# Kernel tuning notes

Measured on AMD Instinct MI355X. Metric: run time of the kernel, lower is better.

Reference implementation:

```python
import jax, jax.numpy as jnp
import numpy as np

N_NODES = 50000
N_EDGES = 800000
NUM_GRAPHS = 128
KS = 5           # kernel_size per pseudo dim
K = KS * KS      # 25 spline weight matrices per layer


def spline_coeff(pseudo):
    """Open linear (degree-1) B-spline basis for 2-D pseudo coords in [0,1].
    Returns dense per-edge coefficients over the K=25 kernel slots: [E, K]."""
    pos = pseudo * (KS - 1)                      # [E,2]
    lo = jnp.clip(jnp.floor(pos).astype(jnp.int32), 0, KS - 2)
    frac = pos - lo.astype(pseudo.dtype)         # [E,2]
    i0, i1 = lo, lo + 1
    w0, w1 = 1.0 - frac, frac
    # 2^dim = 4 corner combinations, flat index = d0 + KS*d1
    idx = jnp.stack([i0[:, 0] + KS * i0[:, 1],
                     i0[:, 0] + KS * i1[:, 1],
                     i1[:, 0] + KS * i0[:, 1],
                     i1[:, 0] + KS * i1[:, 1]], axis=1)            # [E,4]
    w = jnp.stack([w0[:, 0] * w0[:, 1], w0[:, 0] * w1[:, 1],
                   w1[:, 0] * w0[:, 1], w1[:, 0] * w1[:, 1]], axis=1)  # [E,4]
    E = pseudo.shape[0]
    coeff = jnp.zeros((E, K), pseudo.dtype).at[jnp.arange(E)[:, None], idx].add(w)
    return coeff


def spline_conv(x, coeff, src, dst, W, root, bias):
    """SplineConv: gather src feats, spline-weighted transform, scatter-mean to dst,
    plus root weight and bias. x:[N,in], coeff:[E,K], W:[K,in,out]."""
    n = x.shape[0]
    x_src = x[src]                                # [E,in] gather
    m = coeff[:, 0:1] * (x_src @ W[0])            # [E,out]
    for k in range(1, K):                         # fixed small loop over K kernels
        m = m + coeff[:, k:k + 1] * (x_src @ W[k])
    agg = jax.ops.segment_sum(m, dst, num_segments=n)
    cnt = jax.ops.segment_sum(jnp.ones((src.shape[0],), x.dtype), dst, num_segments=n)
    agg = agg / jnp.maximum(cnt, 1.0)[:, None]    # mean aggregation (PyG default)
    return agg + x @ root + bias


def setup_inputs() -> dict:
    key = jax.random.key(0)
    ks = jax.random.split(key, 16)
    s = 0.1  # small init scale for numerical stability
    return {
        "x": jax.random.normal(ks[0], (N_NODES, 1), jnp.float32),
        "position": jax.random.uniform(ks[1], (N_NODES, 2), jnp.float32),
        "pseudo": jax.random.uniform(ks[2], (N_EDGES, 2), jnp.float32),
        "edge_index": jax.random.randint(ks[3], (2, N_EDGES), 0, N_NODES, jnp.int32),
        "batch": jnp.sort(jax.random.randint(ks[4], (N_NODES,), 0, NUM_GRAPHS, jnp.int32)),
        "W1": s * jax.random.normal(ks[5], (K, 1, 32), jnp.float32),
        "root1": s * jax.random.normal(ks[6], (1, 32), jnp.float32),
        "b1": jnp.zeros((32,), jnp.float32),
        "W2": s * jax.random.normal(ks[7], (K, 32, 64), jnp.float32),
        "root2": s * jax.random.normal(ks[8], (32, 64), jnp.float32),
        "b2": jnp.zeros((64,), jnp.float32),
        "W3": s * jax.random.normal(ks[9], (K, 64, 64), jnp.float32),
        "root3": s * jax.random.normal(ks[10], (64, 64), jnp.float32),
        "b3": jnp.zeros((64,), jnp.float32),
        "fc_w": s * jax.random.normal(ks[11], (64, 10), jnp.float32),
        "fc_b": jnp.zeros((10,), jnp.float32),
    }


def reference(x, position, pseudo, edge_index, batch,
              W1, root1, b1, W2, root2, b2, W3, root3, b3, fc_w, fc_b):
    # `position` is accepted but unused, matching the original forward.
    src, dst = edge_index[0], edge_index[1]
    coeff = spline_coeff(pseudo)
    h = jax.nn.elu(spline_conv(x, coeff, src, dst, W1, root1, b1))
    h = jax.nn.elu(spline_conv(h, coeff, src, dst, W2, root2, b2))
    h = jax.nn.elu(spline_conv(h, coeff, src, dst, W3, root3, b3))
    # scatter_mean pooling over batch indices -> [NUM_GRAPHS, 64]
    pooled = jax.ops.segment_sum(h, batch, num_segments=NUM_GRAPHS)
    gcnt = jax.ops.segment_sum(jnp.ones((h.shape[0],), h.dtype), batch,
                               num_segments=NUM_GRAPHS)
    pooled = pooled / jnp.maximum(gcnt, 1.0)[:, None]
    # dropout is identity in eval mode
    logits = pooled @ fc_w + fc_b
    return jax.nn.log_softmax(logits, axis=1)
```

## Files before the change

### kernel.cpp

```cpp
#include <hip/hip_runtime.h>

#define NN 50000
#define NE 800000
#define NG 128
#define NB_SCAN 196
#define PADW 0xC1000000u

typedef unsigned int uint;
typedef unsigned short ushort;
typedef __attribute__((ext_vector_type(8))) short short8;
typedef __attribute__((ext_vector_type(4))) float f32x4;
typedef __attribute__((ext_vector_type(16))) float f32x16;

__device__ __forceinline__ float bf2f(ushort u){ union{uint i; float f;} v; v.i=(uint)u<<16; return v.f; }
__device__ __forceinline__ ushort f2bf(float f){ union{float f; uint i;} v; v.f=f; return (ushort)((v.i + 0x7FFFu + ((v.i>>16)&1u))>>16); }
__device__ __forceinline__ int iswz(int i){ return i ^ ((i>>4)&3); }

__global__ void zero_k(int* hist, float* pooled, int* gcnt){
    int i = blockIdx.x*blockDim.x + threadIdx.x;
    if (i < NN) hist[i] = 0;
    if (i < NG*64) pooled[i] = 0.f;
    if (i < NG) gcnt[i] = 0;
}

__global__ void hist_k(const int* __restrict__ ei, int* __restrict__ hist){
    int e = blockIdx.x*blockDim.x + threadIdx.x;
    if (e < NE) atomicAdd(&hist[ei[NE + e]], 1);
}

__global__ __launch_bounds__(256) void scan1(const int* __restrict__ hist, int* __restrict__ bsum){
    __shared__ int sm[256];
    int t = threadIdx.x, i = blockIdx.x*256 + t;
    sm[t] = (i < NN) ? hist[i] : 0;
    __syncthreads();
    for (int o = 128; o > 0; o >>= 1){ if (t < o) sm[t] += sm[t+o]; __syncthreads(); }
    if (t == 0) bsum[blockIdx.x] = sm[0];
}
__global__ __launch_bounds__(256) void scan2(const int* __restrict__ bsum, int* __restrict__ bpre){
    __shared__ int sm[256];
    int t = threadIdx.x;
    int v = (t < NB_SCAN) ? bsum[t] : 0;
    sm[t] = v; __syncthreads();
    int acc = v;
    for (int o = 1; o < 256; o <<= 1){
        int u = (t >= o) ? sm[t-o] : 0; __syncthreads();
        acc += u; sm[t] = acc; __syncthreads();
    }
    if (t < NB_SCAN) bpre[t] = acc - v;
}
__global__ __launch_bounds__(256) void scan3(const int* __restrict__ hist, const int* __restrict__ bpre,
                                             int* __restrict__ offs, int* __restrict__ cursor,
                                             float* __restrict__ invc){
    __shared__ int sm[256];
    int t = threadIdx.x, b = blockIdx.x, i = b*256 + t;
    int v = (i < NN) ? hist[i] : 0;
    sm[t] = v; __syncthreads();
    int acc = v;
    for (int o = 1; o < 256; o <<= 1){
        int u = (t >= o) ? sm[t-o] : 0; __syncthreads();
        acc += u; sm[t] = acc; __syncthreads();
    }
    int excl = acc - v + bpre[b];
    if (i < NN){ offs[i] = excl; cursor[i] = excl; invc[i] = 1.0f/(float)max(v,1); }
    if (i == NN-1) offs[NN] = NE;
}

__global__ void scatter_k(const int* __restrict__ ei, const float* __restrict__ pseudo,
                          int* __restrict__ cursor, uint4* __restrict__ payA){
    int e = blockIdx.x*blockDim.x + threadIdx.x;
    if (e >= NE) return;
    float2 ps = *(const float2*)(pseudo + 2*(size_t)e);
    float px = ps.x * 4.0f, py = ps.y * 4.0f;
    int lx = min(max((int)floorf(px), 0), 3);
    int ly = min(max((int)floorf(py), 0), 3);
    uint meta = (uint)ei[e] | ((uint)lx<<16) | ((uint)ly<<18);
    int pos = atomicAdd(&cursor[ei[NE + e]], 1);
    payA[pos] = make_uint4(meta, __float_as_uint(px), __float_as_uint(py), 0u);
}

template<int IN>
__global__ void wprep_k(const float* __restrict__ W, const float* __restrict__ root, ushort* __restrict__ Bp){
    const int total = 26*IN*64;
    int tid = blockIdx.x*blockDim.x + threadIdx.x;
    if (tid >= total) return;
    int j    = tid & 7;
    int lane = (tid >> 3) & 63;
    int ctkt = tid >> 9;
    int ct   = ctkt & 3;
    int kt   = ctkt >> 2;
    int kk   = kt*32 + (lane>>4)*8 + j;
    int col  = ct*16 + (lane & 15);
    float v;
    if (kk < 25*IN){ int k = kk / IN; int i = kk % IN; v = W[((size_t)k*IN + i)*64 + col]; }
    else           { v = root[(size_t)(kk - 25*IN)*64 + col]; }
    Bp[tid] = f2bf(v);
}

__global__ __launch_bounds__(256) void reduce1_k(const float* __restrict__ x, const uint4* __restrict__ payA,
                                                 const int* __restrict__ offs, const float* __restrict__ invc,
                                                 const float* __restrict__ W1, const float* __restrict__ root1,
                                                 const float* __restrict__ b1, ushort* __restrict__ h1bf){
    __shared__ float w1s[25*32];
    for (int i = threadIdx.x; i < 25*32; i += 256) w1s[i] = W1[i];
    __syncthreads();
    int wid  = threadIdx.x >> 6;
    int lane = threadIdx.x & 63;
    int o    = lane & 31;
    int half = lane >> 5;
    int d    = blockIdx.x*4 + wid;
    int s = offs[d], e = offs[d+1];
    float acc = 0.f;
#define E1(QA, XS) { uint meta = (QA).x; \
    int lx = (meta>>16)&3, ly = (meta>>18)&3; \
    float px = __uint_as_float((QA).y), py = __uint_as_float((QA).z); \
    float fx = px - (float)lx, fy = py - (float)ly; \
    float gx = 1.f - fx, gy = 1.f - fy; \
    float wa = half ? fx*gy : gx*gy; \
    float wb = half ? fx*fy : gx*fy; \
    int ka = ly*5 + lx + half; \
    acc += (wa*w1s[ka*32 + o] + wb*w1s[(ka+5)*32 + o]) * (XS); }
    int p = s;
    for (; p + 4 <= e; p += 4){
        uint4 a0 = payA[p], a1 = payA[p+1], a2 = payA[p+2], a3 = payA[p+3];
        float x0 = x[a0.x & 0xFFFF], x1 = x[a1.x & 0xFFFF];
        float x2 = x[a2.x & 0xFFFF], x3 = x[a3.x & 0xFFFF];
        E1(a0, x0) E1(a1, x1) E1(a2, x2) E1(a3, x3)
    }
    for (; p < e; ++p){
        uint4 a0 = payA[p];
        float x0 = x[a0.x & 0xFFFF];
        E1(a0, x0)
    }
#undef E1
    acc += __shfl_xor(acc, 32);
    if (half == 0){
        float val = acc*invc[d] + x[d]*root1[o] + b1[o];
        val = val > 0.f ? val : expm1f(val);
        h1bf[(size_t)d*32 + o] = f2bf(val);
    }
}

#define WCALC(Q0, AH, AL) { \
    float px_ = __uint_as_float((Q0).y), py_ = __uint_as_float((Q0).z); \
    float wx_ = fmaxf(1.f - fabsf(px_ - fi0), 0.f); \
    float wy_ = fmaxf(1.f - fabsf(py_ - fj0), 0.f); \
    float wv_ = wx_ * wy_; \
    uint wb_ = __float_as_uint(wv_); \
    (AH) = (short)(ushort)(wb_ >> 16); \
    float hif_ = __uint_as_float(wb_ & 0xFFFF0000u); \
    (AL) = (short)(ushort)(__float_as_uint(wv_ - hif_) >> 16); }

template<int MODE>
__global__ __launch_bounds__(512) void fused32(
        const ushort* __restrict__ hin, const uint4* __restrict__ payA,
        const int* __restrict__ offs, const float* __restrict__ invc,
        const ushort* __restrict__ Bp, const float* __restrict__ bias,
        const int* __restrict__ batch, ushort* __restrict__ hout,
        float* __restrict__ pooled, int* __restrict__ gcnt)
{
    constexpr int KT = 26, KH = 13;
    __shared__ __align__(16) ushort Sb[KT*512];
    __shared__ __align__(16) uint4 eA[8][16];
    __shared__ float red[1024];
    __shared__ float outS[1024];

    const int tid = threadIdx.x, lane = tid & 63, w = tid >> 6;
    const int ln31 = lane & 31, kg2 = lane >> 5;
    const int d0 = blockIdx.x * 16;
    const float fi0 = (float)(ln31 % 5), fj0 = (float)(ln31 / 5);
    const uint4 PAD4 = make_uint4(0u, PADW, PADW, 0u);

    for (int nn = 0; nn < 2; ++nn){
        const int node = w*2 + nn;
        const int d = d0 + node;
        int s = offs[d];
        int h = offs[d+1] - s;
        int steps = (h + 15) >> 4;

        f32x16 accH;
        #pragma unroll
        for (int q = 0; q < 16; ++q) accH[q] = 0.f;

        uint4 vA = PAD4;
        {
            int rem = (h < 16) ? h : 16;
            if (lane < rem) vA = payA[(size_t)s + lane];
        }
        for (int ks = 0; ks < steps; ++ks){
            if (lane < 16) eA[w][lane] = vA;
            if (ks+1 < steps){
                int rem = h - (ks+1)*16; if (rem > 16) rem = 16;
                uint4 nA = PAD4;
                if (lane < rem) nA = payA[(size_t)(s + (ks+1)*16) + lane];
                vA = nA;
            }
            short8 ah, al;
            uint srcs[8];
            #pragma unroll
            for (int j = 0; j < 8; ++j){
                uint4 q0 = eA[w][kg2*8 + j];
                WCALC(q0, ah[j], al[j])
                srcs[j] = q0.x & 0xFFFFu;
            }
            short8 bfv;
            #pragma unroll
            for (int j = 0; j < 8; ++j)
                bfv[j] = (short)hin[(size_t)srcs[j]*32 + ln31];
            accH = __builtin_amdgcn_mfma_f32_32x32x16_bf16(ah, bfv, accH, 0, 0, 0);
            accH = __builtin_amdgcn_mfma_f32_32x32x16_bf16(al, bfv, accH, 0, 0, 0);
        }

        {
            float ic = invc[d];
            int jd  = ln31 & 7;
            int l3  = ln31 >> 3;
            #pragma unroll
            for (int reg = 0; reg < 16; ++reg){
                int r = (reg & 3) + 8*(reg >> 2) + 4*kg2;
                if (r < 25)
                    Sb[r*512 + iswz(l3*16 + node)*8 + jd] = f2bf(accH[reg]*ic);
            }
            if (lane < 32)
                Sb[25*512 + iswz(((lane>>3)&3)*16 + node)*8 + (lane&7)] = hin[(size_t)d*32 + lane];
        }
    }
    __syncthreads();

    {
        int ct = w & 3, kh = w >> 2;
        int c15 = lane & 15, kg = lane >> 4;
        int ig = iswz(lane);
        f32x4 a4 = {0.f,0.f,0.f,0.f};
        const ushort* bb = Bp + ct*512 + (size_t)lane*8;
        #pragma unroll
        for (int k = 0; k < KH; ++k){
            int kt = kh*KH + k;
            short8 a = *(const short8*)(Sb + kt*512 + ig*8);
            short8 b = *(const short8*)(bb + (size_t)kt*2048);
            a4 = __builtin_amdgcn_mfma_f32_16x16x32_bf16(a, b, a4, 0, 0, 0);
        }
        if (kh == 1){
            float* rr = red + (ct*64 + lane)*4;
            rr[0]=a4[0]; rr[1]=a4[1]; rr[2]=a4[2]; rr[3]=a4[3];
        }
        __syncthreads();
        if (kh == 0){
            const float* rr = red + (ct*64 + lane)*4;
            int col = ct*16 + c15;
            float bs = bias[col];
            #pragma unroll
            for (int jq = 0; jq < 4; ++jq){
                int r16 = kg*4 + jq;
                float v = a4[jq] + rr[jq] + bs;
                v = v > 0.f ? v : expm1f(v);
                if (MODE == 0) ((ushort*)outS)[r16*64 + col] = f2bf(v);
                else           outS[r16*64 + col] = v;
            }
        }
    }
    __syncthreads();

    if (MODE == 0){
        uint* dst = (uint*)(hout + (size_t)d0*64);
        dst[tid] = ((const uint*)outS)[tid];
    } else {
        if (w == 0){
            int c = lane;
            float run = 0.f; int gprev = batch[d0];
            for (int r = 0; r < 16; ++r){
                int g = batch[d0 + r];
                if (g != gprev){ atomicAdd(&pooled[gprev*64 + c], run); run = 0.f; gprev = g; }
                run += outS[r*64 + c];
            }
            atomicAdd(&pooled[gprev*64 + c], run);
        } else if (w == 1 && lane == 0){
            int cnt = 0; int gprev = batch[d0];
            for (int r = 0; r < 16; ++r){
                int g = batch[d0 + r];
                if (g != gprev){ atomicAdd(&gcnt[gprev], cnt); cnt = 0; gprev = g; }
                cnt++;
            }
            atomicAdd(&gcnt[gprev], cnt);
        }
    }
}

template<int MODE>
__global__ __launch_bounds__(512) void fused64(
        const ushort* __restrict__ hin, const uint4* __restrict__ payA,
        const int* __restrict__ offs, const float* __restrict__ invc,
        const ushort* __restrict__ Bp, const float* __restrict__ bias,
        const int* __restrict__ batch, ushort* __restrict__ hout,
        float* __restrict__ pooled, int* __restrict__ gcnt)
{
    constexpr int KT = 52, KH = 26;
    __shared__ __align__(16) ushort Sb[KT*512];
    __shared__ __align__(16) uint4 eA[8][16];
    __shared__ float red[1024];
    __shared__ float outS[1024];

    const int tid = threadIdx.x, lane = tid & 63, w = tid >> 6;
    const int ln31 = lane & 31, kg2 = lane >> 5;
    const int d0 = blockIdx.x * 16;
    const float fi0 = (float)(ln31 % 5), fj0 = (float)(ln31 / 5);
    const uint4 PAD4 = make_uint4(0u, PADW, PADW, 0u);

    for (int nn = 0; nn < 2; ++nn){
        const int node = w*2 + nn;
        const int d = d0 + node;
        int s = offs[d];
        int h = offs[d+1] - s;
        int steps = (h + 15) >> 4;

        f32x16 acc0, acc1;
        #pragma unroll
        for (int q = 0; q < 16; ++q){ acc0[q] = 0.f; acc1[q] = 0.f; }

        uint4 vA = PAD4;
        {
            int rem = (h < 16) ? h : 16;
            if (lane < rem) vA = payA[(size_t)s + lane];
        }
        for (int ks = 0; ks < steps; ++ks){
            if (lane < 16) eA[w][lane] = vA;
            if (ks+1 < steps){
                int rem = h - (ks+1)*16; if (rem > 16) rem = 16;
                uint4 nA = PAD4;
                if (lane < rem) nA = payA[(size_t)(s + (ks+1)*16) + lane];
                vA = nA;
            }
            short8 ah, al;
            uint hx[8];
            #pragma unroll
            for (int j = 0; j < 8; ++j){
                uint4 q0 = eA[w][kg2*8 + j];
                WCALC(q0, ah[j], al[j])
                hx[j] = *(const uint*)(hin + (size_t)(q0.x & 0xFFFFu)*64 + 2*ln31);
            }
            short8 b0, b1;
            #pragma unroll
            for (int j = 0; j < 8; ++j){
                b0[j] = (short)(ushort)hx[j];
                b1[j] = (short)(ushort)(hx[j] >> 16);
            }
            acc0 = __builtin_amdgcn_mfma_f32_32x32x16_bf16(ah, b0, acc0, 0, 0, 0);
            acc0 = __builtin_amdgcn_mfma_f32_32x32x16_bf16(al, b0, acc0, 0, 0, 0);
            acc1 = __builtin_amdgcn_mfma_f32_32x32x16_bf16(ah, b1, acc1, 0, 0, 0);
            acc1 = __builtin_amdgcn_mfma_f32_32x32x16_bf16(al, b1, acc1, 0, 0, 0);
        }

        {
            float ic = invc[d];
            int off0 = 2*ln31;
            int fhi  = ln31 >> 4;
            int kgp  = (off0 >> 3) & 3;
            int jd0  = off0 & 7;
            int gsl  = iswz(kgp*16 + node)*8;
            #pragma unroll
            for (int reg = 0; reg < 16; ++reg){
                int r = (reg & 3) + 8*(reg >> 2) + 4*kg2;
                if (r < 25){
                    int kt = r*2 + fhi;
                    uint pk = (uint)f2bf(acc0[reg]*ic) | ((uint)f2bf(acc1[reg]*ic) << 16);
                    *(uint*)(Sb + kt*512 + gsl + jd0) = pk;
                }
            }
            int f = lane;
            Sb[(50 + (f>>5))*512 + iswz(((f>>3)&3)*16 + node)*8 + (f&7)] = hin[(size_t)d*64 + f];
        }
    }
    __syncthreads();

    {
        int ct = w & 3, kh = w >> 2;
        int c15 = lane & 15, kg = lane >> 4;
        int ig = iswz(lane);
        f32x4 a4 = {0.f,0.f,0.f,0.f};
        const ushort* bb = Bp + ct*512 + (size_t)lane*8;
        #pragma unroll
        for (int k = 0; k < KH; ++k){
            int kt = kh*KH + k;
            short8 a = *(const short8*)(Sb + kt*512 + ig*8);
            short8 b = *(const short8*)(bb + (size_t)kt*2048);
            a4 = __builtin_amdgcn_mfma_f32_16x16x32_bf16(a, b, a4, 0, 0, 0);
        }
        if (kh == 1){
            float* rr = red + (ct*64 + lane)*4;
            rr[0]=a4[0]; rr[1]=a4[1]; rr[2]=a4[2]; rr[3]=a4[3];
        }
        __syncthreads();
        if (kh == 0){
            const float* rr = red + (ct*64 + lane)*4;
            int col = ct*16 + c15;
            float bs = bias[col];
            #pragma unroll
            for (int jq = 0; jq < 4; ++jq){
                int r16 = kg*4 + jq;
                float v = a4[jq] + rr[jq] + bs;
                v = v > 0.f ? v : expm1f(v);
                if (MODE == 0) ((ushort*)outS)[r16*64 + col] = f2bf(v);
                else           outS[r16*64 + col] = v;
            }
        }
    }
    __syncthreads();

    if (MODE == 0){
        uint* dst = (uint*)(hout + (size_t)d0*64);
        dst[tid] = ((const uint*)outS)[tid];
    } else {
        if (w == 0){
            int c = lane;
            float run = 0.f; int gprev = batch[d0];
            for (int r = 0; r < 16; ++r){
                int g = batch[d0 + r];
                if (g != gprev){ atomicAdd(&pooled[gprev*64 + c], run); run = 0.f; gprev = g; }
                run += outS[r*64 + c];
            }
            atomicAdd(&pooled[gprev*64 + c], run);
        } else if (w == 1 && lane == 0){
            int cnt = 0; int gprev = batch[d0];
            for (int r = 0; r < 16; ++r){
                int g = batch[d0 + r];
                if (g != gprev){ atomicAdd(&gcnt[gprev], cnt); cnt = 0; gprev = g; }
                cnt++;
            }
            atomicAdd(&gcnt[gprev], cnt);
        }
    }
}

__global__ __launch_bounds__(128) void head_k(const float* __restrict__ pooled, const int* __restrict__ gcnt,
                                              const float* __restrict__ fcw, const float* __restrict__ fcb,
                                              float* __restrict__ out){
    int g = threadIdx.x;
    if (g >= NG) return;
    float inv = 1.0f / fmaxf((float)gcnt[g], 1.0f);
    float logits[10];
    #pragma unroll
    for (int c = 0; c < 10; ++c) logits[c] = fcb[c];
    for (int o = 0; o < 64; ++o){
        float m = pooled[g*64 + o] * inv;
        #pragma unroll
        for (int c = 0; c < 10; ++c) logits[c] += m * fcw[o*10 + c];
    }
    float mx = logits[0];
    #pragma unroll
    for (int c = 1; c < 10; ++c) mx = fmaxf(mx, logits[c]);
    float ssum = 0.f;
    #pragma unroll
    for (int c = 0; c < 10; ++c) ssum += expf(logits[c] - mx);
    float lse = logf(ssum) + mx;
    #pragma unroll
    for (int c = 0; c < 10; ++c) out[g*10 + c] = logits[c] - lse;
}

extern "C" void kernel_launch(void* const* d_in, const int* in_sizes, int n_in,
                              void* d_out, int out_size, void* d_ws, size_t ws_size,
                              hipStream_t stream) {
    const float* x      = (const float*)d_in[0];
    const float* pseudo = (const float*)d_in[2];
    const int*   ei     = (const int*)  d_in[3];
    const int*   batch  = (const int*)  d_in[4];
    const float* W1     = (const float*)d_in[5];
    const float* root1  = (const float*)d_in[6];
    const float* b1     = (const float*)d_in[7];
    const float* W2     = (const float*)d_in[8];
    const float* root2  = (const float*)d_in[9];
    const float* b2     = (const float*)d_in[10];
    const float* W3     = (const float*)d_in[11];
    const float* root3  = (const float*)d_in[12];
    const float* b3     = (const float*)d_in[13];
    const float* fcw    = (const float*)d_in[14];
    const float* fcb    = (const float*)d_in[15];
    float* out = (float*)d_out;

    char* ws = (char*)d_ws;
    size_t off = 0;
    auto alloc = [&](size_t bytes)->char*{ char* p = ws + off; off += (bytes + 255) / 256 * 256; return p; };
    uint4*  payA   = (uint4*) alloc((size_t)NE*16);
    ushort* h1bf   = (ushort*)alloc((size_t)NN*32*2);
    ushort* h2bf   = (ushort*)alloc((size_t)NN*64*2);
    int*    hist   = (int*)   alloc((size_t)NN*4);
    int*    offs   = (int*)   alloc((size_t)(NN+1)*4);
    int*    cursor = (int*)   alloc((size_t)NN*4);
    float*  invc   = (float*) alloc((size_t)NN*4);
    int*    bsum   = (int*)   alloc((size_t)NB_SCAN*4);
    int*    bpre   = (int*)   alloc((size_t)NB_SCAN*4);
    ushort* Bp2    = (ushort*)alloc((size_t)26*2048*2);
    ushort* Bp3    = (ushort*)alloc((size_t)52*2048*2);
    float*  pooled = (float*) alloc((size_t)NG*64*4);
    int*    gcnt   = (int*)   alloc((size_t)NG*4);
    (void)ws_size; (void)in_sizes; (void)n_in; (void)out_size;

    zero_k   <<<NB_SCAN, 256, 0, stream>>>(hist, pooled, gcnt);
    hist_k   <<<(NE+255)/256, 256, 0, stream>>>(ei, hist);
    scan1    <<<NB_SCAN, 256, 0, stream>>>(hist, bsum);
    scan2    <<<1, 256, 0, stream>>>(bsum, bpre);
    scan3    <<<NB_SCAN, 256, 0, stream>>>(hist, bpre, offs, cursor, invc);
    scatter_k<<<(NE+255)/256, 256, 0, stream>>>(ei, pseudo, cursor, payA);
    wprep_k<32><<<(26*32*64 + 255)/256, 256, 0, stream>>>(W2, root2, Bp2);
    wprep_k<64><<<(26*64*64 + 255)/256, 256, 0, stream>>>(W3, root3, Bp3);
    reduce1_k<<<NN/4, 256, 0, stream>>>(x, payA, offs, invc, W1, root1, b1, h1bf);
    fused32<0><<<NN/16, 512, 0, stream>>>(h1bf, payA, offs, invc, Bp2, b2, batch, h2bf, pooled, gcnt);
    fused64<1><<<NN/16, 512, 0, stream>>>(h2bf, payA, offs, invc, Bp3, b3, batch, h2bf, pooled, gcnt);
    head_k   <<<1, 128, 0, stream>>>(pooled, gcnt, fcw, fcb, out);
}
```

Before: 280.3 us.

## Double-buffer edge payload via direct global-to-LDS async loads

Replaces the register-staged edge payload prefetch with global_load_lds DMA into a double-buffered LDS array per wave. The next 16-edge chunk is issued before processing the current one, with explicit vmcnt waits and a scheduling barrier. The goal is to drop the register round-trip and the LDS store, and to overlap payload fetch with the gather and MFMA work. The manual waitcnt and the lack of explicit LDS visibility sync add correctness risk, and the sched_barrier may limit compiler interleaving of the gather loads.

```diff
diff --git a/kernel.cpp b/kernel.cpp
--- a/kernel.cpp
+++ b/kernel.cpp
@@ -150,6 +150,15 @@
     float hif_ = __uint_as_float(wb_ & 0xFFFF0000u); \
     (AL) = (short)(ushort)(__float_as_uint(wv_ - hif_) >> 16); }
 
+#define STAGE(BUF, STEP) { \
+    int rem_ = h - (STEP)*16; if (rem_ > 16) rem_ = 16; \
+    if (lane < 16 && lane >= rem_) eA[w][BUF][lane] = PAD4; \
+    if (lane < rem_){ \
+        __builtin_amdgcn_global_load_lds( \
+            (const __attribute__((address_space(1))) void*)(payA + (size_t)s + (STEP)*16 + lane), \
+            (__attribute__((address_space(3))) void*)&eA[w][BUF][lane], 16, 0, 0); \
+    } }
+
 template<int MODE>
 __global__ __launch_bounds__(512) void fused32(
         const ushort* __restrict__ hin, const uint4* __restrict__ payA,
@@ -160,7 +169,7 @@
 {
     constexpr int KT = 26, KH = 13;
     __shared__ __align__(16) ushort Sb[KT*512];
-    __shared__ __align__(16) uint4 eA[8][16];
+    __shared__ __align__(16) uint4 eA[8][2][16];
     __shared__ float red[1024];
     __shared__ float outS[1024];
 
@@ -181,31 +190,23 @@
         #pragma unroll
         for (int q = 0; q < 16; ++q) accH[q] = 0.f;
 
-        uint4 vA = PAD4;
-        {
-            int rem = (h < 16) ? h : 16;
-            if (lane < rem) vA = payA[(size_t)s + lane];
-        }
+        if (steps > 0) STAGE(0, 0)
         for (int ks = 0; ks < steps; ++ks){
-            if (lane < 16) eA[w][lane] = vA;
+            int cb = ks & 1;
             if (ks+1 < steps){
-                int rem = h - (ks+1)*16; if (rem > 16) rem = 16;
-                uint4 nA = PAD4;
-                if (lane < rem) nA = payA[(size_t)(s + (ks+1)*16) + lane];
-                vA = nA;
-            }
-            short8 ah, al;
-            uint srcs[8];
+                STAGE(cb^1, ks+1)
+                asm volatile("s_waitcnt vmcnt(1)" ::: "memory");
+            } else {
+                asm volatile("s_waitcnt vmcnt(0)" ::: "memory");
+            }
+            __builtin_amdgcn_sched_barrier(0);
+            short8 ah, al; short8 bfv;
             #pragma unroll
             for (int j = 0; j < 8; ++j){
-                uint4 q0 = eA[w][kg2*8 + j];
+                uint4 q0 = eA[w][cb][kg2*8 + j];
                 WCALC(q0, ah[j], al[j])
-                srcs[j] = q0.x & 0xFFFFu;
-            }
-            short8 bfv;
-            #pragma unroll
-            for (int j = 0; j < 8; ++j)
-                bfv[j] = (short)hin[(size_t)srcs[j]*32 + ln31];
+                bfv[j] = (short)hin[(size_t)(q0.x & 0xFFFFu)*32 + ln31];
+            }
             accH = __builtin_amdgcn_mfma_f32_32x32x16_bf16(ah, bfv, accH, 0, 0, 0);
             accH = __builtin_amdgcn_mfma_f32_32x32x16_bf16(al, bfv, accH, 0, 0, 0);
         }
@@ -295,7 +296,7 @@
 {
     constexpr int KT = 52, KH = 26;
     __shared__ __align__(16) ushort Sb[KT*512];
-    __shared__ __align__(16) uint4 eA[8][16];
+    __shared__ __align__(16) uint4 eA[8][2][16];
     __shared__ float red[1024];
     __shared__ float outS[1024];
 
@@ -316,24 +317,20 @@
         #pragma unroll
         for (int q = 0; q < 16; ++q){ acc0[q] = 0.f; acc1[q] = 0.f; }
 
-        uint4 vA = PAD4;
-        {
-            int rem = (h < 16) ? h : 16;
-            if (lane < rem) vA = payA[(size_t)s + lane];
-        }
+        if (steps > 0) STAGE(0, 0)
         for (int ks = 0; ks < steps; ++ks){
-            if (lane < 16) eA[w][lane] = vA;
+            int cb = ks & 1;
             if (ks+1 < steps){
-                int rem = h - (ks+1)*16; if (rem > 16) rem = 16;
-                uint4 nA = PAD4;
-                if (lane < rem) nA = payA[(size_t)(s + (ks+1)*16) + lane];
-                vA = nA;
-            }
-            short8 ah, al;
-            uint hx[8];
+                STAGE(cb^1, ks+1)
+                asm volatile("s_waitcnt vmcnt(1)" ::: "memory");
+            } else {
+                asm volatile("s_waitcnt vmcnt(0)" ::: "memory");
+            }
+            __builtin_amdgcn_sched_barrier(0);
+            short8 ah, al; uint hx[8];
             #pragma unroll
             for (int j = 0; j < 8; ++j){
-                uint4 q0 = eA[w][kg2*8 + j];
+                uint4 q0 = eA[w][cb][kg2*8 + j];
                 WCALC(q0, ah[j], al[j])
                 hx[j] = *(const uint*)(hin + (size_t)(q0.x & 0xFFFFu)*64 + 2*ln31);
             }
```

After: 277.1 us, median of 2. Within noise of the previous version (-1.1%).
